# Kernel optimization log

Measured on AMD Instinct MI355X. Metric: run time of the kernel, lower is better.

## Reference

```python
import jax, jax.numpy as jnp
import numpy as np

NUM_EXPERTS = 4


def _conv1x1(w, b, x):
    # w: [out,in], b: [out], x: [B,in,H,W]
    return jnp.einsum('oc,bchw->bohw', w, x) + b[None, :, None, None]


def _sobel(x):
    c = x.shape[1]
    kx = jnp.array([[-1., 0., 1.], [-2., 0., 2.], [-1., 0., 1.]], dtype=x.dtype)
    ky = jnp.array([[-1., -2., -1.], [0., 0., 0.], [1., 2., 1.]], dtype=x.dtype)
    wx = jnp.broadcast_to(kx[None, None], (c, 1, 3, 3))
    wy = jnp.broadcast_to(ky[None, None], (c, 1, 3, 3))
    dn = ('NCHW', 'OIHW', 'NCHW')
    gx = jax.lax.conv_general_dilated(x, wx, (1, 1), [(1, 1), (1, 1)],
                                      dimension_numbers=dn, feature_group_count=c)
    gy = jax.lax.conv_general_dilated(x, wy, (1, 1), [(1, 1), (1, 1)],
                                      dimension_numbers=dn, feature_group_count=c)
    return gx, gy


def _bilinear_sample(x, gx, gy):
    # torch F.grid_sample(mode='bilinear', padding_mode='zeros', align_corners=False)
    # x: [B,C,H,W]; gx, gy: [B,Hs,Ws] normalized coords in [-1,1]
    B, C, H, W = x.shape
    ix = ((gx + 1.0) * W - 1.0) * 0.5
    iy = ((gy + 1.0) * H - 1.0) * 0.5
    x0 = jnp.floor(ix)
    y0 = jnp.floor(iy)
    wx1 = ix - x0
    wx0 = 1.0 - wx1
    wy1 = iy - y0
    wy0 = 1.0 - wy1
    xf = x.reshape(B, C, H * W)

    def gather(xc, yc):
        valid = (xc >= 0) & (xc <= W - 1) & (yc >= 0) & (yc <= H - 1)
        xi = jnp.clip(xc, 0, W - 1).astype(jnp.int32)
        yi = jnp.clip(yc, 0, H - 1).astype(jnp.int32)
        idx = yi * W + xi  # [B,Hs,Ws]
        v = jax.vmap(lambda xb, ib: xb[:, ib])(xf, idx)  # [B,C,Hs,Ws]
        return v * valid[:, None].astype(x.dtype)

    return (gather(x0, y0) * (wx0 * wy0)[:, None]
            + gather(x0 + 1, y0) * (wx1 * wy0)[:, None]
            + gather(x0, y0 + 1) * (wx0 * wy1)[:, None]
            + gather(x0 + 1, y0 + 1) * (wx1 * wy1)[:, None])


def _forward(x, wc_e, we_e, wb1, bb1, wb2, bb2, wr, br, wo, bo, wcv, bcv, scale, scale2):
    B, c, h, w = x.shape
    sh = round(h * scale)
    sw = round(w * scale2)

    grad_x, grad_y = _sobel(x)

    # relative-offset coordinate embedding, [1,4,sh,sw]
    ih = (jnp.arange(sh, dtype=x.dtype) + 0.5) / scale
    coor_h = ih - jnp.floor(ih + 0.001) - 0.5  # [sh]
    iw = (jnp.arange(sw, dtype=x.dtype) + 0.5) / scale2
    coor_w = iw - jnp.floor(iw + 0.001) - 0.5  # [sw]
    inp = jnp.stack([
        jnp.full((sh, sw), 1.0 / scale2, dtype=x.dtype),
        jnp.full((sh, sw), 1.0 / scale, dtype=x.dtype),
        jnp.broadcast_to(coor_h[:, None], (sh, sw)),
        jnp.broadcast_to(coor_w[None, :], (sh, sw)),
    ], axis=0)[None]

    emb = jax.nn.relu(_conv1x1(wb2, bb2, jax.nn.relu(_conv1x1(wb1, bb1, inp))))
    offset = _conv1x1(wo, bo, emb)                 # [1,2,sh,sw]
    routing = jax.nn.sigmoid(_conv1x1(wr, br, emb))  # [1,E,sh,sw]

    # per-pixel soft mixture of expert compress/expand matrices
    rw = routing.reshape(NUM_EXPERTS, sh * sw).T   # [N,E]
    wc = (rw @ wc_e.reshape(NUM_EXPERTS, -1)).reshape(sh, sw, c // 8, c)
    we = (rw @ we_e.reshape(NUM_EXPERTS, -1)).reshape(sh, sw, c, c // 8)

    feat = _conv1x1(wcv, bcv, jnp.concatenate([x, grad_x, grad_y], axis=1))  # [B,64,h,w]

    # base grid (align_corners=True-style normalization, as in the source) + learned offsets
    gx0 = ((jnp.arange(sw, dtype=x.dtype) + 0.5) / scale2 - 0.5) * 2.0 / (w - 1) - 1.0
    gy0 = ((jnp.arange(sh, dtype=x.dtype) + 0.5) / scale - 0.5) * 2.0 / (h - 1) - 1.0
    gx = jnp.broadcast_to(gx0[None, None, :] + offset[:, 0] * (2.0 / (w - 1)), (B, sh, sw))
    gy = jnp.broadcast_to(gy0[None, :, None] + offset[:, 1] * (2.0 / (h - 1)), (B, sh, sw))

    fea0 = _bilinear_sample(feat, gx, gy)          # [B,64,sh,sw]

    mid = jnp.einsum('hwkc,bchw->bhwk', wc, fea0)  # per-pixel compress (k=C//8)
    out = jnp.einsum('hwck,bhwk->bchw', we, mid)   # per-pixel expand
    return out + fea0


def setup_inputs() -> dict:
    key = jax.random.key(0)
    ks = jax.random.split(key, 13)
    s = 0.05
    return {
        'x': jax.random.normal(ks[0], (2, 64, 192, 192), jnp.float32),
        'weight_compress': jax.random.normal(ks[1], (4, 8, 64), jnp.float32) * s,
        'weight_expand': jax.random.normal(ks[2], (4, 64, 8), jnp.float32) * s,
        'w_body1': jax.random.normal(ks[3], (64, 4), jnp.float32) * s,
        'b_body1': jax.random.normal(ks[4], (64,), jnp.float32) * s,
        'w_body2': jax.random.normal(ks[5], (64, 64), jnp.float32) * s,
        'b_body2': jax.random.normal(ks[6], (64,), jnp.float32) * s,
        'w_routing': jax.random.normal(ks[7], (4, 64), jnp.float32) * s,
        'b_routing': jax.random.normal(ks[8], (4,), jnp.float32) * s,
        'w_offset': jax.random.normal(ks[9], (2, 64), jnp.float32) * s,
        'b_offset': jax.random.normal(ks[10], (2,), jnp.float32) * s,
        'w_conv': jax.random.normal(ks[11], (64, 192), jnp.float32) * s,
        'b_conv': jax.random.normal(ks[12], (64,), jnp.float32) * s,
        'scale': 2,
        'scale2': 2,
    }


def reference(x, weight_compress, weight_expand, w_body1, b_body1, w_body2, b_body2,
              w_routing, b_routing, w_offset, b_offset, w_conv, b_conv, scale, scale2):
    return _forward(x, weight_compress, weight_expand, w_body1, b_body1, w_body2, b_body2,
                    w_routing, b_routing, w_offset, b_offset, w_conv, b_conv, scale, scale2)
```

## Files before the change

kernel.cpp:

```cpp
#include <hip/hip_runtime.h>
#include <hip/hip_bf16.h>
#include <math.h>

#define BN  2
#define CN  64
#define HN  192
#define WN  192
#define SH  384
#define SW  384
#define HW  (HN * WN)
#define NPIX (BN * HN * WN)

typedef __attribute__((ext_vector_type(8))) short bf16x8;
typedef __attribute__((ext_vector_type(4))) float f32x4;

#define CPAD  72
#define MAINB (BN * HN * 3)
#define TBLB  64

__device__ inline unsigned short f2bf(float f) {
    unsigned int u = __float_as_uint(f);
    u += 0x7fffu + ((u >> 16) & 1u);
    return (unsigned short)(u >> 16);
}
__device__ inline unsigned int pkbf(float a, float b) {
    return (unsigned int)f2bf(a) | ((unsigned int)f2bf(b) << 16);
}

__device__ inline void run_mlp(int lane, float in0, float in1, float chv, float cwv,
    const float* __restrict__ wb1, const float* __restrict__ bb1,
    const float* __restrict__ wb2, const float* __restrict__ bb2,
    const float* __restrict__ wr,  const float* __restrict__ wo, float p[6])
{
    float4 w1 = ((const float4*)wb1)[lane];
    float h1 = fmaxf(bb1[lane] + w1.x * in0 + w1.y * in1 + w1.z * chv + w1.w * cwv, 0.f);
    const float4* w2row = (const float4*)(wb2 + lane * 64);
    float acc = bb2[lane];
#pragma unroll
    for (int q = 0; q < 16; ++q) {
        float4 wv = w2row[q];
        acc += wv.x * __shfl(h1, q * 4 + 0)
             + wv.y * __shfl(h1, q * 4 + 1)
             + wv.z * __shfl(h1, q * 4 + 2)
             + wv.w * __shfl(h1, q * 4 + 3);
    }
    float h2 = fmaxf(acc, 0.f);
#pragma unroll
    for (int e = 0; e < 4; ++e) p[e] = wr[e * 64 + lane] * h2;
#pragma unroll
    for (int e = 0; e < 2; ++e) p[4 + e] = wo[e * 64 + lane] * h2;
#pragma unroll
    for (int m = 1; m < 64; m <<= 1) {
#pragma unroll
        for (int e = 0; e < 6; ++e) p[e] += __shfl_xor(p[e], m);
    }
}

__global__ __launch_bounds__(256) void feat_table_kernel(
    const float* __restrict__ x,
    const float* __restrict__ wcv,
    const float* __restrict__ bcv,
    float* __restrict__ feat,
    const float* __restrict__ wb1, const float* __restrict__ bb1,
    const float* __restrict__ wb2, const float* __restrict__ bb2,
    const float* __restrict__ wr,  const float* __restrict__ br,
    const float* __restrict__ wo,  const float* __restrict__ bo,
    const float* __restrict__ wce, const float* __restrict__ wee,
    const int* __restrict__ scale_p, const int* __restrict__ scale2_p,
    float* __restrict__ tblEntry, unsigned short* __restrict__ tblM)
{
    __shared__ __attribute__((aligned(16))) unsigned short smem_u16[3 * 66 * CPAD];

    int tid  = threadIdx.x;
    int lane = tid & 63;

    if (blockIdx.x >= MAINB) {
        float* wcmL = (float*)smem_u16;
        float* wemL = wcmL + 1024;
        float* reL  = wemL + 1024;

        int sc = scale_p[0], sc2 = scale2_p[0];
        float scale = (float)sc, scale2 = (float)sc2;
        float in0 = 1.f / scale2, in1 = 1.f / scale;
        bool fast = (sc2 == 2 && sc <= 16);
        int tb = blockIdx.x - MAINB;

        if (fast) {
            int pi = tb;
            if (pi >= sc) return;
            if (tid < 64) {
                float ih = (pi + 0.5f) / scale;
                float chv = ih - floorf(ih + 0.001f) - 0.5f;
                float p0[6], p1[6];
                {
                    float iw = 0.5f / scale2;
                    float cwv = iw - floorf(iw + 0.001f) - 0.5f;
                    run_mlp(lane, in0, in1, chv, cwv, wb1, bb1, wb2, bb2, wr, wo, p0);
                }
                {
                    float iw = 1.5f / scale2;
                    float cwv = iw - floorf(iw + 0.001f) - 0.5f;
                    run_mlp(lane, in0, in1, chv, cwv, wb1, bb1, wb2, bb2, wr, wo, p1);
                }
                if (lane == 0) {
                    float* t0 = tblEntry + (pi * 2 + 0) * 8;
                    float* t1 = tblEntry + (pi * 2 + 1) * 8;
#pragma unroll
                    for (int e = 0; e < 4; ++e) {
                        float rE = 1.f / (1.f + expf(-(p0[e] + br[e])));
                        float rO = 1.f / (1.f + expf(-(p1[e] + br[e])));
                        t0[e] = rE; t1[e] = rO;
                        reL[e] = rE; reL[4 + e] = rO;
                    }
                    t0[4] = p0[4] + bo[0]; t0[5] = p0[5] + bo[1];
                    t1[4] = p1[4] + bo[0]; t1[5] = p1[5] + bo[1];
                }
            }
            __syncthreads();
            float reE0 = reL[0], reE1 = reL[1], reE2 = reL[2], reE3 = reL[3];
            float reO0 = reL[4], reO1 = reL[5], reO2 = reL[6], reO3 = reL[7];
            for (int idx = tid; idx < 512; idx += 256) {
                float a = wce[idx], bq = wce[512 + idx], c = wce[1024 + idx], d = wce[1536 + idx];
                wcmL[idx]       = reE0 * a + reE1 * bq + reE2 * c + reE3 * d;
                wcmL[512 + idx] = reO0 * a + reO1 * bq + reO2 * c + reO3 * d;
                float e_ = wee[idx], f = wee[512 + idx], g = wee[1024 + idx], h = wee[1536 + idx];
                wemL[idx]       = reE0 * e_ + reE1 * f + reE2 * g + reE3 * h;
                wemL[512 + idx] = reO0 * e_ + reO1 * f + reO2 * g + reO3 * h;
            }
            __syncthreads();
            int co  = tid >> 2;
            int ci0 = (tid & 3) << 4;
            float w0[8], w1[8];
#pragma unroll
            for (int k = 0; k < 8; ++k) {
                w0[k] = wemL[co * 8 + k];
                w1[k] = wemL[512 + co * 8 + k];
            }
            unsigned short* tbp = tblM + (size_t)pi * 2 * 4096;
#pragma unroll
            for (int cc = 0; cc < 16; ++cc) {
                int ci = ci0 + cc;
                float m0 = 0.f, m1 = 0.f;
#pragma unroll
                for (int k = 0; k < 8; ++k) {
                    m0 += w0[k] * wcmL[k * 64 + ci];
                    m1 += w1[k] * wcmL[512 + k * 64 + ci];
                }
                tbp[co * 64 + ci]        = f2bf(0.5f * (m0 + m1));
                tbp[4096 + co * 64 + ci] = f2bf(0.5f * (m0 - m1));
            }
        } else {
            int w_ = (tb * 256 + tid) >> 6;
            if (w_ >= sc * sc2) return;
            int pi = w_ / sc2, pj = w_ - pi * sc2;
            float ih = (pi + 0.5f) / scale;
            float chv = ih - floorf(ih + 0.001f) - 0.5f;
            float iw = (pj + 0.5f) / scale2;
            float cwv = iw - floorf(iw + 0.001f) - 0.5f;
            float p[6];
            run_mlp(lane, in0, in1, chv, cwv, wb1, bb1, wb2, bb2, wr, wo, p);
            if (lane == 0) {
                float* tp = tblEntry + w_ * 8;
#pragma unroll
                for (int e = 0; e < 4; ++e) tp[e] = 1.f / (1.f + expf(-(p[e] + br[e])));
                tp[4] = p[4] + bo[0];
                tp[5] = p[5] + bo[1];
            }
        }
        return;
    }

    int bi = blockIdx.x;
    int jt = bi % 3;
    int t2 = bi / 3;
    int i0 = t2 % HN;
    int b  = t2 / HN;
    int j0 = jt * 64;
    int w  = __builtin_amdgcn_readfirstlane(tid >> 6);

    int row = lane & 15;
    int q   = lane >> 4;

    const float KXc[9] = {-1.f, 0.f, 1.f, -2.f, 0.f, 2.f, -1.f, 0.f, 1.f};
    const float KYc[9] = {-1.f, -2.f, -1.f, 0.f, 0.f, 0.f, 1.f, 2.f, 1.f};
    bf16x8 afrag[9][2];
    {
        int o = (w << 4) + row;
        const float* wp = wcv + o * 192;
        float v0[2][8], v1[2][8], v2[2][8];
#pragma unroll
        for (int kc = 0; kc < 2; ++kc) {
            int kb = kc * 32 + q * 8;
            float4 a0 = *(const float4*)(wp + kb);
            float4 a1 = *(const float4*)(wp + kb + 4);
            float4 b0 = *(const float4*)(wp + 64 + kb);
            float4 b1 = *(const float4*)(wp + 64 + kb + 4);
            float4 c0 = *(const float4*)(wp + 128 + kb);
            float4 c1 = *(const float4*)(wp + 128 + kb + 4);
            v0[kc][0]=a0.x; v0[kc][1]=a0.y; v0[kc][2]=a0.z; v0[kc][3]=a0.w;
            v0[kc][4]=a1.x; v0[kc][5]=a1.y; v0[kc][6]=a1.z; v0[kc][7]=a1.w;
            v1[kc][0]=b0.x; v1[kc][1]=b0.y; v1[kc][2]=b0.z; v1[kc][3]=b0.w;
            v1[kc][4]=b1.x; v1[kc][5]=b1.y; v1[kc][6]=b1.z; v1[kc][7]=b1.w;
            v2[kc][0]=c0.x; v2[kc][1]=c0.y; v2[kc][2]=c0.z; v2[kc][3]=c0.w;
            v2[kc][4]=c1.x; v2[kc][5]=c1.y; v2[kc][6]=c1.z; v2[kc][7]=c1.w;
        }
#pragma unroll
        for (int t = 0; t < 9; ++t) {
#pragma unroll
            for (int kc = 0; kc < 2; ++kc) {
                bf16x8 a;
#pragma unroll
                for (int e = 0; e < 8; ++e) {
                    float f = v1[kc][e] * KXc[t] + v2[kc][e] * KYc[t];
                    if (t == 4) f += v0[kc][e];
                    a[e] = (short)f2bf(f);
                }
                afrag[t][kc] = a;
            }
        }
    }

    if (tid < 3 * 66) {
        int rowi = tid / 66;
        int col  = tid - rowi * 66;
        int sr = i0 - 1 + rowi;
        bool rok = (sr >= 0) && (sr < HN);
        int src = rok ? sr : 0;
        int hc = j0 - 1 + col;
        bool cok = (hc >= 0) && (hc < WN);
        int hcc = cok ? hc : 0;
        float msk = (rok && cok) ? 1.f : 0.f;
        const float* p = x + (size_t)b * CN * HW + (size_t)src * WN + hcc;
        unsigned short* xrow = smem_u16 + (rowi * 66 + col) * CPAD;
#pragma unroll 4
        for (int k = 0; k < 8; ++k) {
            float a0 = p[0]              * msk;
            float a1 = p[(size_t)HW]     * msk;
            float a2 = p[2 * (size_t)HW] * msk;
            float a3 = p[3 * (size_t)HW] * msk;
            float a4 = p[4 * (size_t)HW] * msk;
            float a5 = p[5 * (size_t)HW] * msk;
            float a6 = p[6 * (size_t)HW] * msk;
            float a7 = p[7 * (size_t)HW] * msk;
            uint4 uu;
            uu.x = pkbf(a0, a1);
            uu.y = pkbf(a2, a3);
            uu.z = pkbf(a4, a5);
            uu.w = pkbf(a6, a7);
            *(uint4*)(xrow + (k << 3)) = uu;
            p += 8 * (size_t)HW;
        }
    }

    __syncthreads();

    f32x4 acc[4] = {};
    const unsigned short* bb0 = smem_u16 + row * CPAD + (q << 3);
#pragma unroll
    for (int nt = 0; nt < 4; ++nt) {
#pragma unroll
        for (int t = 0; t < 9; ++t) {
            int a_ = t / 3, dxi = t - a_ * 3;
#pragma unroll
            for (int kc = 0; kc < 2; ++kc) {
                bf16x8 bv = *(const bf16x8*)(bb0 + (a_ * 66 + nt * 16 + dxi) * CPAD + kc * 32);
                acc[nt] = __builtin_amdgcn_mfma_f32_16x16x32_bf16(afrag[t][kc], bv, acc[nt], 0, 0, 0);
            }
        }
    }

    size_t rb0 = (size_t)b * CN * HW + (size_t)i0 * WN + j0 + row;
#pragma unroll
    for (int rr = 0; rr < 4; ++rr) {
        int oc = (w << 4) + q * 4 + rr;
        float bias = bcv[oc];
        size_t rowb = rb0 + (size_t)oc * HW;
#pragma unroll
        for (int nt = 0; nt < 4; ++nt)
            feat[rowb + nt * 16] = acc[nt][rr] + bias;
    }
}

#define BKP 72
__global__ __launch_bounds__(256) void out_kernel(
    const float* __restrict__ feat,
    const float* __restrict__ tblEntry,
    const unsigned short* __restrict__ tblM,
    const float* __restrict__ wce,
    const float* __restrict__ wee,
    const int* __restrict__ scale_p, const int* __restrict__ scale2_p,
    float* __restrict__ out)
{
    __shared__ __attribute__((aligned(16))) float smem[64 * 65 + 64 * (BKP / 2)];
    float* fea32 = smem;
    unsigned short* Bsv = (unsigned short*)(smem + 64 * 65);
    float* midp = smem;

    int Bk = blockIdx.x;
    int T = gridDim.x;
    int t = ((T & 7) == 0) ? ((Bk & 7) * (T >> 3) + (Bk >> 3)) : Bk;

    int tid = threadIdx.x;
    int g = __builtin_amdgcn_readfirstlane(tid >> 6);
    int lane = tid & 63;
    int pix0 = t * 64;
    int b = pix0 / (SH * SW);
    int r0 = pix0 - b * SH * SW;
    int i = r0 / SW;
    int j0 = r0 - i * SW;
    int j = j0 + lane;
    int r = r0 + lane;

    int sc = scale_p[0], sc2 = scale2_p[0];
    float scale = (float)sc, scale2 = (float)sc2;
    int pi = i - (i / sc) * sc;
    int pj = j - (j / sc2) * sc2;
    int entry = pi * sc2 + pj;
    float offx = tblEntry[entry * 8 + 4];
    float offy = tblEntry[entry * 8 + 5];

    const float inv_wm1 = 2.f / (float)(WN - 1);
    const float inv_hm1 = 2.f / (float)(HN - 1);
    float gx = ((j + 0.5f) / scale2 - 0.5f) * inv_wm1 - 1.f + offx * inv_wm1;
    float gy = ((i + 0.5f) / scale  - 0.5f) * inv_hm1 - 1.f + offy * inv_hm1;

    float ix = ((gx + 1.f) * WN - 1.f) * 0.5f;
    float iy = ((gy + 1.f) * HN - 1.f) * 0.5f;
    float fx0 = floorf(ix), fy0 = floorf(iy);
    int x0 = (int)fx0, y0 = (int)fy0;
    float wx1 = ix - fx0, wx0 = 1.f - wx1;
    float wy1 = iy - fy0, wy0 = 1.f - wy1;

    bool vx0 = (x0 >= 0) && (x0 <= WN - 1);
    bool vx1 = (x0 + 1 >= 0) && (x0 + 1 <= WN - 1);
    bool vy0 = (y0 >= 0) && (y0 <= HN - 1);
    bool vy1 = (y0 + 1 >= 0) && (y0 + 1 <= HN - 1);
    bool v00 = vx0 && vy0, v10 = vx1 && vy0, v01 = vx0 && vy1, v11 = vx1 && vy1;
    float w00 = wx0 * wy0, w10 = wx1 * wy0, w01 = wx0 * wy1, w11 = wx1 * wy1;

    int i00 = y0 * WN + x0;
    int i10 = i00 + 1;
    int i01 = i00 + WN;
    int i11 = i01 + 1;

    const float* fb = feat + (size_t)b * CN * HW;

    float f0[16];
#pragma unroll
    for (int cc = 0; cc < 16; ++cc) {
        const float* fc = fb + (size_t)(g * 16 + cc) * HW;
        float a  = v00 ? fc[i00] : 0.f;
        float bq = v10 ? fc[i10] : 0.f;
        float cq = v01 ? fc[i01] : 0.f;
        float dq = v11 ? fc[i11] : 0.f;
        f0[cc] = a * w00 + bq * w10 + cq * w01 + dq * w11;
    }

    bool fast = (sc2 == 2 && sc <= 16);
    if (fast) {
        int px = lane;
#pragma unroll
        for (int cc = 0; cc < 16; ++cc)
            fea32[px * 65 + g * 16 + cc] = f0[cc];
#pragma unroll
        for (int cc = 0; cc < 16; cc += 2) {
            unsigned int pk = (unsigned int)f2bf(f0[cc]) | ((unsigned int)f2bf(f0[cc + 1]) << 16);
            *(unsigned int*)(Bsv + px * BKP + g * 16 + cc) = pk;
        }

        int row = lane & 15;
        int kb  = (lane >> 4) << 3;
        const unsigned short* Mb = tblM + (size_t)pi * 2 * 4096 + (g * 16 + row) * 64 + kb;
        bf16x8 a1[2], a2[2];
        a1[0] = *(const bf16x8*)(Mb);
        a1[1] = *(const bf16x8*)(Mb + 32);
        a2[0] = *(const bf16x8*)(Mb + 4096);
        a2[1] = *(const bf16x8*)(Mb + 4096 + 32);

        __syncthreads();

        f32x4 acc1[4] = {}, acc2[4] = {};
        const unsigned short* bp = Bsv + (lane & 15) * BKP + kb;
#pragma unroll
        for (int nt = 0; nt < 4; ++nt) {
            const unsigned short* bnt = bp + nt * 16 * BKP;
#pragma unroll
            for (int ks = 0; ks < 2; ++ks) {
                bf16x8 bf = *(const bf16x8*)(bnt + ks * 32);
                acc1[nt] = __builtin_amdgcn_mfma_f32_16x16x32_bf16(a1[ks], bf, acc1[nt], 0, 0, 0);
                acc2[nt] = __builtin_amdgcn_mfma_f32_16x16x32_bf16(a2[ks], bf, acc2[nt], 0, 0, 0);
            }
        }

        int q = lane >> 4;
#pragma unroll
        for (int rr = 0; rr < 4; ++rr) {
            int c = g * 16 + q * 4 + rr;
            size_t rowb = (size_t)(b * CN + c) * SH * SW + r0;
#pragma unroll
            for (int nt = 0; nt < 4; ++nt) {
                int n = (lane & 15) + nt * 16;
                float sgn = (n & 1) ? -1.f : 1.f;
                float v = fea32[n * 65 + c] + acc1[nt][rr] + sgn * acc2[nt][rr];
                out[rowb + n] = v;
            }
        }
    } else {
        float4 rw = *(const float4*)(tblEntry + entry * 8);
        float re[4] = {rw.x, rw.y, rw.z, rw.w};
        float part[4][8];
#pragma unroll
        for (int e = 0; e < 4; ++e) {
#pragma unroll
            for (int k = 0; k < 8; ++k) {
                const float* wrow = wce + (e * 8 + k) * 64 + g * 16;
                float d = 0.f;
#pragma unroll
                for (int cc = 0; cc < 16; ++cc) d += wrow[cc] * f0[cc];
                part[e][k] = d;
            }
        }
#pragma unroll
        for (int k = 0; k < 8; ++k) {
            float m = re[0] * part[0][k] + re[1] * part[1][k]
                    + re[2] * part[2][k] + re[3] * part[3][k];
            midp[(g * 64 + lane) * 9 + k] = m;
        }
        __syncthreads();
        float mid[8];
#pragma unroll
        for (int k = 0; k < 8; ++k)
            mid[k] = midp[(0 * 64 + lane) * 9 + k] + midp[(1 * 64 + lane) * 9 + k]
                   + midp[(2 * 64 + lane) * 9 + k] + midp[(3 * 64 + lane) * 9 + k];
#pragma unroll
        for (int cc = 0; cc < 16; ++cc) {
            int c = g * 16 + cc;
            float v = f0[cc];
#pragma unroll
            for (int e = 0; e < 4; ++e) {
                const float* wrow = wee + (e * 64 + c) * 8;
                float d = 0.f;
#pragma unroll
                for (int k = 0; k < 8; ++k) d += wrow[k] * mid[k];
                v += re[e] * d;
            }
            out[(size_t)(b * CN + c) * SH * SW + r] = v;
        }
    }
}

extern "C" void kernel_launch(void* const* d_in, const int* in_sizes, int n_in,
                              void* d_out, int out_size, void* d_ws, size_t ws_size,
                              hipStream_t stream) {
    const float* x    = (const float*)d_in[0];
    const float* wce  = (const float*)d_in[1];
    const float* wee  = (const float*)d_in[2];
    const float* wb1  = (const float*)d_in[3];
    const float* bb1  = (const float*)d_in[4];
    const float* wb2  = (const float*)d_in[5];
    const float* bb2  = (const float*)d_in[6];
    const float* wr   = (const float*)d_in[7];
    const float* br   = (const float*)d_in[8];
    const float* wo   = (const float*)d_in[9];
    const float* bo   = (const float*)d_in[10];
    const float* wcv  = (const float*)d_in[11];
    const float* bcv  = (const float*)d_in[12];
    const int*   scale  = (const int*)d_in[13];
    const int*   scale2 = (const int*)d_in[14];
    float* out = (float*)d_out;

    float* feat     = (float*)d_ws;
    float* tblEntry = feat + (size_t)BN * CN * HW;
    unsigned short* tblM = (unsigned short*)(tblEntry + 256 * 8);

    feat_table_kernel<<<MAINB + TBLB, 256, 0, stream>>>(
        x, wcv, bcv, feat, wb1, bb1, wb2, bb2, wr, br, wo, bo,
        wce, wee, scale, scale2, tblEntry, tblM);
    out_kernel<<<BN * SH * SW / 64, 256, 0, stream>>>(feat, tblEntry, tblM,
                                                      wce, wee, scale, scale2, out);
}
```

Before: 152.8 us.

## Split feature conv into prepass with channel-last bf16 transpose and precomputed weight fragments

A new prepass kernel transposes x from NCHW fp32 into a channel-last bf16 buffer, and one block builds the fused Sobel/conv MFMA A-fragments once into a global table. The feature conv kernel then loads its halo tile with coalesced 16-byte reads from the transposed buffer and reads the weight fragments directly, instead of doing strided per-channel gathers and recomputing the fragments in every block. The cost is an extra kernel launch and an extra round trip of x through global memory.

```diff
diff --git a/kernel.cpp b/kernel.cpp
--- a/kernel.cpp
+++ b/kernel.cpp
@@ -15,7 +15,7 @@
 typedef __attribute__((ext_vector_type(4))) float f32x4;
 
 #define CPAD  72
-#define MAINB (BN * HN * 3)
+#define TRB   (BN * HN * 3)
 #define TBLB  64
 
 __device__ inline unsigned short f2bf(float f) {
@@ -56,26 +56,95 @@
     }
 }
 
-__global__ __launch_bounds__(256) void feat_table_kernel(
+__global__ __launch_bounds__(256) void prepass_kernel(
     const float* __restrict__ x,
     const float* __restrict__ wcv,
-    const float* __restrict__ bcv,
-    float* __restrict__ feat,
     const float* __restrict__ wb1, const float* __restrict__ bb1,
     const float* __restrict__ wb2, const float* __restrict__ bb2,
     const float* __restrict__ wr,  const float* __restrict__ br,
     const float* __restrict__ wo,  const float* __restrict__ bo,
     const float* __restrict__ wce, const float* __restrict__ wee,
     const int* __restrict__ scale_p, const int* __restrict__ scale2_p,
+    unsigned short* __restrict__ xt,
+    unsigned short* __restrict__ tblW,
     float* __restrict__ tblEntry, unsigned short* __restrict__ tblM)
 {
-    __shared__ __attribute__((aligned(16))) unsigned short smem_u16[3 * 66 * CPAD];
+    __shared__ __attribute__((aligned(16))) unsigned short sm[64 * CPAD];
 
     int tid  = threadIdx.x;
     int lane = tid & 63;
-
-    if (blockIdx.x >= MAINB) {
-        float* wcmL = (float*)smem_u16;
+    int bi = blockIdx.x;
+
+    if (bi < TRB) {
+        int jt = bi % 3;
+        int t2 = bi / 3;
+        int i  = t2 % HN;
+        int b  = t2 / HN;
+        int j0 = jt * 64;
+        int w  = tid >> 6;
+        int c0 = w * 16;
+
+        const float* xp = x + (size_t)b * CN * HW + (size_t)i * WN + j0 + lane;
+#pragma unroll
+        for (int k = 0; k < 16; k += 2) {
+            float f0 = xp[(size_t)(c0 + k) * HW];
+            float f1 = xp[(size_t)(c0 + k + 1) * HW];
+            *(unsigned int*)(sm + lane * CPAD + c0 + k) = pkbf(f0, f1);
+        }
+        __syncthreads();
+        size_t obase = (((size_t)b * HN + i) * WN + j0) * 64;
+#pragma unroll
+        for (int it = 0; it < 2; ++it) {
+            int task = tid + it * 256;
+            int jj = task >> 3, oc = task & 7;
+            uint4 v = *(const uint4*)(sm + jj * CPAD + oc * 8);
+            *(uint4*)(xt + obase + (size_t)jj * 64 + oc * 8) = v;
+        }
+        return;
+    }
+
+    if (bi == TRB) {
+        const float KXc[9] = {-1.f, 0.f, 1.f, -2.f, 0.f, 2.f, -1.f, 0.f, 1.f};
+        const float KYc[9] = {-1.f, -2.f, -1.f, 0.f, 0.f, 0.f, 1.f, 2.f, 1.f};
+        int wv = tid >> 6;
+        int o  = (wv << 4) + (lane & 15);
+        const float* wp = wcv + o * 192;
+        float v0[2][8], v1[2][8], v2[2][8];
+#pragma unroll
+        for (int kc = 0; kc < 2; ++kc) {
+            int kb = kc * 32 + (lane >> 4) * 8;
+            float4 a0 = *(const float4*)(wp + kb);
+            float4 a1 = *(const float4*)(wp + kb + 4);
+            float4 b0 = *(const float4*)(wp + 64 + kb);
+            float4 b1 = *(const float4*)(wp + 64 + kb + 4);
+            float4 c0 = *(const float4*)(wp + 128 + kb);
+            float4 c1 = *(const float4*)(wp + 128 + kb + 4);
+            v0[kc][0]=a0.x; v0[kc][1]=a0.y; v0[kc][2]=a0.z; v0[kc][3]=a0.w;
+            v0[kc][4]=a1.x; v0[kc][5]=a1.y; v0[kc][6]=a1.z; v0[kc][7]=a1.w;
+            v1[kc][0]=b0.x; v1[kc][1]=b0.y; v1[kc][2]=b0.z; v1[kc][3]=b0.w;
+            v1[kc][4]=b1.x; v1[kc][5]=b1.y; v1[kc][6]=b1.z; v1[kc][7]=b1.w;
+            v2[kc][0]=c0.x; v2[kc][1]=c0.y; v2[kc][2]=c0.z; v2[kc][3]=c0.w;
+            v2[kc][4]=c1.x; v2[kc][5]=c1.y; v2[kc][6]=c1.z; v2[kc][7]=c1.w;
+        }
+#pragma unroll
+        for (int t = 0; t < 9; ++t) {
+#pragma unroll
+            for (int kc = 0; kc < 2; ++kc) {
+                bf16x8 a;
+#pragma unroll
+                for (int e = 0; e < 8; ++e) {
+                    float f = v1[kc][e] * KXc[t] + v2[kc][e] * KYc[t];
+                    if (t == 4) f += v0[kc][e];
+                    a[e] = (short)f2bf(f);
+                }
+                *(bf16x8*)(void*)(tblW + (size_t)(((wv * 9 + t) * 2 + kc) * 64 + lane) * 8) = a;
+            }
+        }
+        return;
+    }
+
+    {
+        float* wcmL = (float*)sm;
         float* wemL = wcmL + 1024;
         float* reL  = wemL + 1024;
 
@@ -83,7 +152,7 @@
         float scale = (float)sc, scale2 = (float)sc2;
         float in0 = 1.f / scale2, in1 = 1.f / scale;
         bool fast = (sc2 == 2 && sc <= 16);
-        int tb = blockIdx.x - MAINB;
+        int tb = bi - (TRB + 1);
 
         if (fast) {
             int pi = tb;
@@ -167,9 +236,19 @@
                 tp[5] = p[5] + bo[1];
             }
         }
-        return;
-    }
-
+    }
+}
+
+__global__ __launch_bounds__(256) void feat_kernel(
+    const unsigned short* __restrict__ xt,
+    const unsigned short* __restrict__ tblW,
+    const float* __restrict__ bcv,
+    float* __restrict__ feat)
+{
+    __shared__ __attribute__((aligned(16))) unsigned short sm[198 * CPAD];
+
+    int tid  = threadIdx.x;
+    int lane = tid & 63;
     int bi = blockIdx.x;
     int jt = bi % 3;
     int t2 = bi / 3;
@@ -181,81 +260,37 @@
     int row = lane & 15;
     int q   = lane >> 4;
 
-    const float KXc[9] = {-1.f, 0.f, 1.f, -2.f, 0.f, 2.f, -1.f, 0.f, 1.f};
-    const float KYc[9] = {-1.f, -2.f, -1.f, 0.f, 0.f, 0.f, 1.f, 2.f, 1.f};
     bf16x8 afrag[9][2];
-    {
-        int o = (w << 4) + row;
-        const float* wp = wcv + o * 192;
-        float v0[2][8], v1[2][8], v2[2][8];
-#pragma unroll
-        for (int kc = 0; kc < 2; ++kc) {
-            int kb = kc * 32 + q * 8;
-            float4 a0 = *(const float4*)(wp + kb);
-            float4 a1 = *(const float4*)(wp + kb + 4);
-            float4 b0 = *(const float4*)(wp + 64 + kb);
-            float4 b1 = *(const float4*)(wp + 64 + kb + 4);
-            float4 c0 = *(const float4*)(wp + 128 + kb);
-            float4 c1 = *(const float4*)(wp + 128 + kb + 4);
-            v0[kc][0]=a0.x; v0[kc][1]=a0.y; v0[kc][2]=a0.z; v0[kc][3]=a0.w;
-            v0[kc][4]=a1.x; v0[kc][5]=a1.y; v0[kc][6]=a1.z; v0[kc][7]=a1.w;
-            v1[kc][0]=b0.x; v1[kc][1]=b0.y; v1[kc][2]=b0.z; v1[kc][3]=b0.w;
-            v1[kc][4]=b1.x; v1[kc][5]=b1.y; v1[kc][6]=b1.z; v1[kc][7]=b1.w;
-            v2[kc][0]=c0.x; v2[kc][1]=c0.y; v2[kc][2]=c0.z; v2[kc][3]=c0.w;
-            v2[kc][4]=c1.x; v2[kc][5]=c1.y; v2[kc][6]=c1.z; v2[kc][7]=c1.w;
-        }
-#pragma unroll
-        for (int t = 0; t < 9; ++t) {
-#pragma unroll
-            for (int kc = 0; kc < 2; ++kc) {
-                bf16x8 a;
-#pragma unroll
-                for (int e = 0; e < 8; ++e) {
-                    float f = v1[kc][e] * KXc[t] + v2[kc][e] * KYc[t];
-                    if (t == 4) f += v0[kc][e];
-                    a[e] = (short)f2bf(f);
-                }
-                afrag[t][kc] = a;
-            }
-        }
-    }
-
-    if (tid < 3 * 66) {
-        int rowi = tid / 66;
-        int col  = tid - rowi * 66;
-        int sr = i0 - 1 + rowi;
-        bool rok = (sr >= 0) && (sr < HN);
-        int src = rok ? sr : 0;
-        int hc = j0 - 1 + col;
-        bool cok = (hc >= 0) && (hc < WN);
-        int hcc = cok ? hc : 0;
-        float msk = (rok && cok) ? 1.f : 0.f;
-        const float* p = x + (size_t)b * CN * HW + (size_t)src * WN + hcc;
-        unsigned short* xrow = smem_u16 + (rowi * 66 + col) * CPAD;
-#pragma unroll 4
-        for (int k = 0; k < 8; ++k) {
-            float a0 = p[0]              * msk;
-            float a1 = p[(size_t)HW]     * msk;
-            float a2 = p[2 * (size_t)HW] * msk;
-            float a3 = p[3 * (size_t)HW] * msk;
-            float a4 = p[4 * (size_t)HW] * msk;
-            float a5 = p[5 * (size_t)HW] * msk;
-            float a6 = p[6 * (size_t)HW] * msk;
-            float a7 = p[7 * (size_t)HW] * msk;
-            uint4 uu;
-            uu.x = pkbf(a0, a1);
-            uu.y = pkbf(a2, a3);
-            uu.z = pkbf(a4, a5);
-            uu.w = pkbf(a6, a7);
-            *(uint4*)(xrow + (k << 3)) = uu;
-            p += 8 * (size_t)HW;
+#pragma unroll
+    for (int t = 0; t < 9; ++t)
+#pragma unroll
+        for (int kc = 0; kc < 2; ++kc)
+            afrag[t][kc] = *(const bf16x8*)(void*)(
+                tblW + (size_t)(((w * 9 + t) * 2 + kc) * 64 + lane) * 8);
+
+#pragma unroll
+    for (int it = 0; it < 7; ++it) {
+        int task = tid + it * 256;
+        if (task < 198 * 8) {
+            int p  = task >> 3;
+            int oc = task & 7;
+            int rowi = p / 66;
+            int col  = p - rowi * 66;
+            int sr = i0 - 1 + rowi;
+            int hc = j0 - 1 + col;
+            bool ok = (sr >= 0) && (sr < HN) && (hc >= 0) && (hc < WN);
+            int srb = ok ? sr : 0;
+            int hcb = ok ? hc : 0;
+            uint4 v = *(const uint4*)(xt + (((size_t)b * HN + srb) * WN + hcb) * 64 + oc * 8);
+            if (!ok) v = (uint4){0u, 0u, 0u, 0u};
+            *(uint4*)(sm + p * CPAD + oc * 8) = v;
         }
     }
 
     __syncthreads();
 
     f32x4 acc[4] = {};
-    const unsigned short* bb0 = smem_u16 + row * CPAD + (q << 3);
+    const unsigned short* bb0 = sm + row * CPAD + (q << 3);
 #pragma unroll
     for (int nt = 0; nt < 4; ++nt) {
 #pragma unroll
@@ -471,11 +506,14 @@
 
     float* feat     = (float*)d_ws;
     float* tblEntry = feat + (size_t)BN * CN * HW;
-    unsigned short* tblM = (unsigned short*)(tblEntry + 256 * 8);
-
-    feat_table_kernel<<<MAINB + TBLB, 256, 0, stream>>>(
-        x, wcv, bcv, feat, wb1, bb1, wb2, bb2, wr, br, wo, bo,
-        wce, wee, scale, scale2, tblEntry, tblM);
+    unsigned short* tblM = (unsigned short*)(tblEntry + 2048);
+    unsigned short* tblW = tblM + 16 * 2 * 4096;
+    unsigned short* xt   = tblW + 4 * 9 * 2 * 64 * 8;
+
+    prepass_kernel<<<TRB + 1 + TBLB, 256, 0, stream>>>(
+        x, wcv, wb1, bb1, wb2, bb2, wr, br, wo, bo,
+        wce, wee, scale, scale2, xt, tblW, tblEntry, tblM);
+    feat_kernel<<<TRB, 256, 0, stream>>>(xt, tblW, bcv, feat);
     out_kernel<<<BN * SH * SW / 64, 256, 0, stream>>>(feat, tblEntry, tblM,
                                                       wce, wee, scale, scale2, out);
 }
```

Result: no change. 155.3 us (+1.6%).
